# Optimization experiments

Measured on AMD Instinct MI355X. Metric: run time of the kernel, lower is better.

The kernel has to match this reference:

```python
import jax, jax.numpy as jnp
import numpy as np

L = 10      # LSTM layers
H = 128     # hidden size
ENC = 4096  # traffic_encoder_output_len
B = 8192    # batch
T = 12      # points_to_predict
NUM_MODES = 25


def setup_inputs() -> dict:
    key = jax.random.key(0)
    ks = jax.random.split(key, 10)
    s = 1.0 / np.sqrt(H)
    return {
        "backbone_encoded": jax.random.normal(ks[0], (B, ENC), jnp.float32),
        "fc_in_W": jax.random.normal(ks[1], (H, ENC), jnp.float32) / np.sqrt(ENC),
        "fc_in_b": jax.random.normal(ks[2], (H,), jnp.float32) * s,
        "Wih": jax.random.normal(ks[3], (L, 4 * H, H), jnp.float32) * s,
        "Whh": jax.random.normal(ks[4], (L, 4 * H, H), jnp.float32) * s,
        "bih": jax.random.normal(ks[5], (L, 4 * H), jnp.float32) * s,
        "bhh": jax.random.normal(ks[6], (L, 4 * H), jnp.float32) * s,
        "fc_out_W": jax.random.normal(ks[7], (3 * NUM_MODES, H), jnp.float32) * s,
        "fc_out_b": jax.random.normal(ks[8], (3 * NUM_MODES,), jnp.float32) * s,
        "points_to_predict": T,
    }


def _lstm_stack(x, Wih, Whh, bih, bhh):
    # x: [B, T, H]; PyTorch gate order: i, f, g, o
    def run_layer(x, l):
        def step(carry, xt):
            h, c = carry
            gates = xt @ Wih[l].T + h @ Whh[l].T + bih[l] + bhh[l]  # [B, 4H]
            i, f, g, o = jnp.split(gates, 4, axis=-1)
            c = jax.nn.sigmoid(f) * c + jax.nn.sigmoid(i) * jnp.tanh(g)
            h = jax.nn.sigmoid(o) * jnp.tanh(c)
            return (h, c), h
        b = x.shape[0]
        h0 = jnp.zeros((b, H), x.dtype)
        _, ys = jax.lax.scan(step, (h0, h0), jnp.swapaxes(x, 0, 1))  # [T, B, H]
        return jnp.swapaxes(ys, 0, 1)

    for l in range(L):
        x = run_layer(x, l)
    return x


def reference(backbone_encoded, fc_in_W, fc_in_b, Wih, Whh, bih, bhh,
              fc_out_W, fc_out_b, points_to_predict):
    enc = jax.nn.relu(backbone_encoded @ fc_in_W.T + fc_in_b)        # [B, H]
    x = jnp.repeat(enc[:, None, :], points_to_predict, axis=1)      # [B, T, H]
    y = _lstm_stack(x, Wih, Whh, bih, bhh)                           # [B, T, H]
    fc = y @ fc_out_W.T + fc_out_b                                   # [B, T, 75]
    b, t, _ = fc.shape
    # chunk(25, dim=channels) of consecutive pairs -> [B, 25, T, 2]
    predictions = fc[:, :, :50].reshape(b, t, NUM_MODES, 2).transpose(0, 2, 1, 3)
    probabilities = jax.nn.softmax(fc[:, -1, 50:], axis=-1)          # [B, 25]
    return predictions, probabilities
```

## Files before the change

### kernel.cpp

```cpp
#include <hip/hip_runtime.h>

typedef _Float16 h16;
typedef _Float16 h8 __attribute__((ext_vector_type(8)));
typedef float f4 __attribute__((ext_vector_type(4)));

#define NB 8192
#define NENC 4096
#define NH 128
#define NL 10
#define NT 12

#define OFF_FCIN 0
#define SZ_FCIN (128*4096)
#define OFF_W (OFF_FCIN + SZ_FCIN)
#define SZ_W (10*2*512*128)
#define OFF_FCOUT (OFF_W + SZ_W)
#define SZ_FCOUT (80*128)
#define OFF_ENC (OFF_FCOUT + SZ_FCOUT)
#define SZ_ENC (8192*128)
#define BYTE_BIAS ((OFF_ENC + SZ_ENC)*2)

__device__ __forceinline__ float sigf(float x) {
  float e = __builtin_amdgcn_exp2f(-1.4426950408889634f * x);
  return __builtin_amdgcn_rcpf(1.0f + e);
}
__device__ __forceinline__ float tanhf_(float x) {
  float e = __builtin_amdgcn_exp2f(-2.8853900817779268f * x);
  return 2.0f * __builtin_amdgcn_rcpf(1.0f + e) - 1.0f;
}
__device__ __forceinline__ f4 splat4(float v) { f4 r; r[0]=v; r[1]=v; r[2]=v; r[3]=v; return r; }
__device__ __forceinline__ h8 cvt8(float4 a, float4 b) {
  h8 r; r[0]=(h16)a.x; r[1]=(h16)a.y; r[2]=(h16)a.z; r[3]=(h16)a.w;
  r[4]=(h16)b.x; r[5]=(h16)b.y; r[6]=(h16)b.z; r[7]=(h16)b.w; return r;
}

__global__ __launch_bounds__(256) void prep(const float* __restrict__ fcinW,
                                            const float* __restrict__ Wih,
                                            const float* __restrict__ Whh,
                                            const float* __restrict__ bih,
                                            const float* __restrict__ bhh,
                                            const float* __restrict__ fcoutW,
                                            h16* __restrict__ wsh,
                                            float* __restrict__ wbias) {
  int idx = blockIdx.x * 256 + threadIdx.x;
  if (idx < 65536) {
    int r = idx >> 9, k8 = idx & 511;
    const float* src = fcinW + r * 4096 + k8 * 8;
    h8 v = cvt8(*(const float4*)src, *(const float4*)(src + 4));
    *(h8*)(wsh + OFF_FCIN + (((r >> 4) * 512 + k8) * 128 + (r & 15) * 8)) = v;
  } else if (idx < 229376) {
    int rel = idx - 65536;
    int l = rel >> 14, rr = rel & 16383;
    int ssel = rr >> 13, rk8 = rr & 8191;
    int r = rk8 >> 4, k8 = rk8 & 15;
    const float* src = (ssel ? Whh : Wih) + l * 65536 + r * 128 + k8 * 8;
    h8 v = cvt8(*(const float4*)src, *(const float4*)(src + 4));
    *(h8*)(wsh + OFF_W + (l * 2 + ssel) * 65536 +
           (((r >> 4) * 16 + k8) * 128 + (r & 15) * 8)) = v;
  } else if (idx < 230656) {
    int rel = idx - 229376;
    int r = rel >> 4, k8 = rel & 15;
    h8 v;
    if (r < 75) {
      const float* src = fcoutW + r * 128 + k8 * 8;
      v = cvt8(*(const float4*)src, *(const float4*)(src + 4));
    } else {
      for (int j = 0; j < 8; ++j) v[j] = (h16)0.f;
    }
    *(h8*)(wsh + OFF_FCOUT + (((r >> 4) * 16 + k8) * 128 + (r & 15) * 8)) = v;
  } else if (idx < 235776) {
    int rel = idx - 230656;
    wbias[rel] = bih[rel] + bhh[rel];
  }
}

__global__ __launch_bounds__(256) void kin(const float* __restrict__ A,
                                           const float* __restrict__ bvec,
                                           h16* __restrict__ wsh) {
  const h16* Wp = wsh + OFF_FCIN;
  h16* ench = wsh + OFF_ENC;
  int tid = threadIdx.x;
  int w = tid >> 6, lane = tid & 63, s = lane & 15, q = lane >> 4;
  int m0 = blockIdx.x * 16;
  int c0 = w * 32 + s, c1 = c0 + 16;
  f4 acc0 = splat4(bvec[c0]);
  f4 acc1 = splat4(bvec[c1]);
  const float* arow = A + (size_t)(m0 + s) * NENC;
  const h16* wp0 = Wp + (w * 2 + 0) * (512 * 128) + s * 8;
  const h16* wp1 = Wp + (w * 2 + 1) * (512 * 128) + s * 8;
#pragma unroll 4
  for (int kb = 0; kb < 128; ++kb) {
    int k0 = kb * 32 + q * 8;
    float4 x0 = *(const float4*)(arow + k0);
    float4 x1 = *(const float4*)(arow + k0 + 4);
    h8 af = cvt8(x0, x1);
    h8 b0 = *(const h8*)(wp0 + (kb * 4 + q) * 128);
    h8 b1 = *(const h8*)(wp1 + (kb * 4 + q) * 128);
    acc0 = __builtin_amdgcn_mfma_f32_16x16x32_f16(af, b0, acc0, 0, 0, 0);
    acc1 = __builtin_amdgcn_mfma_f32_16x16x32_f16(af, b1, acc1, 0, 0, 0);
  }
#pragma unroll
  for (int r = 0; r < 4; ++r) {
    int b = m0 + q * 4 + r;
    float v0 = acc0[r]; v0 = v0 > 0.f ? v0 : 0.f;
    float v1 = acc1[r]; v1 = v1 > 0.f ? v1 : 0.f;
    ench[(size_t)b * NH + c0] = (h16)v0;
    ench[(size_t)b * NH + c1] = (h16)v1;
  }
}

__global__ __launch_bounds__(512, 2) void lstm(h16* __restrict__ wsh,
                                               const float* __restrict__ wbias,
                                               const float* __restrict__ fcoutb,
                                               float* __restrict__ out) {
  __shared__ h16 xbuf[NT][32][136];
  __shared__ h16 hbuf[2][32][136];
  int tid = threadIdx.x;
  int w = tid >> 6, lane = tid & 63, s = lane & 15, q = lane >> 4;
  int brow = blockIdx.x * 32;
  const h16* ench = wsh + OFF_ENC;
  {
    int r = tid >> 4, cg = (tid & 15) * 8;
    h8 e = *(const h8*)(ench + (size_t)(brow + r) * NH + cg);
#pragma unroll
    for (int t = 0; t < NT; ++t) *(h8*)&xbuf[t][r][cg] = e;
  }
  h8 wx[4][4], wh[4][4];
  float bb[4];
  float c[2][4];
  for (int l = 0; l < NL; ++l) {
    const h16* wih = wsh + OFF_W + (l * 2 + 0) * 65536;
    const h16* whh = wsh + OFF_W + (l * 2 + 1) * 65536;
#pragma unroll
    for (int g = 0; g < 4; ++g) {
#pragma unroll
      for (int kt = 0; kt < 4; ++kt) {
        int off = (((g * 8 + w) * 16 + kt * 4 + q) * 128) + s * 8;
        wx[g][kt] = *(const h8*)(wih + off);
        wh[g][kt] = *(const h8*)(whh + off);
      }
      bb[g] = wbias[l * 512 + g * 128 + w * 16 + s];
    }
#pragma unroll
    for (int mt = 0; mt < 2; ++mt)
#pragma unroll
      for (int r = 0; r < 4; ++r) c[mt][r] = 0.f;
    for (int j = tid; j < 32 * 136 / 2; j += 512) ((unsigned int*)hbuf)[j] = 0u;
    __syncthreads();
    for (int t = 0; t < NT; ++t) {
      int cur = t & 1, nxt = cur ^ 1;
      f4 acc[4][2];
#pragma unroll
      for (int g = 0; g < 4; ++g)
#pragma unroll
        for (int mt = 0; mt < 2; ++mt) acc[g][mt] = splat4(bb[g]);
#pragma unroll
      for (int mt = 0; mt < 2; ++mt) {
        h8 ax[4], ah[4];
#pragma unroll
        for (int kt = 0; kt < 4; ++kt) {
          ax[kt] = *(const h8*)&xbuf[t][mt * 16 + s][kt * 32 + q * 8];
          ah[kt] = *(const h8*)&hbuf[cur][mt * 16 + s][kt * 32 + q * 8];
        }
#pragma unroll
        for (int g = 0; g < 4; ++g)
#pragma unroll
          for (int kt = 0; kt < 4; ++kt) {
            acc[g][mt] = __builtin_amdgcn_mfma_f32_16x16x32_f16(ax[kt], wx[g][kt], acc[g][mt], 0, 0, 0);
            acc[g][mt] = __builtin_amdgcn_mfma_f32_16x16x32_f16(ah[kt], wh[g][kt], acc[g][mt], 0, 0, 0);
          }
      }
      h16 hv[2][4];
#pragma unroll
      for (int mt = 0; mt < 2; ++mt)
#pragma unroll
        for (int r = 0; r < 4; ++r) {
          float iv = acc[0][mt][r], fv = acc[1][mt][r];
          float gv = acc[2][mt][r], ov = acc[3][mt][r];
          float cc = sigf(fv) * c[mt][r] + sigf(iv) * tanhf_(gv);
          c[mt][r] = cc;
          hv[mt][r] = (h16)(sigf(ov) * tanhf_(cc));
        }
      __syncthreads();
#pragma unroll
      for (int mt = 0; mt < 2; ++mt)
#pragma unroll
        for (int r = 0; r < 4; ++r) {
          int row = mt * 16 + q * 4 + r, col = w * 16 + s;
          xbuf[t][row][col] = hv[mt][r];
          hbuf[nxt][row][col] = hv[mt][r];
        }
      __syncthreads();
    }
  }
  h8 wo[5][4];
  float bo[5];
  const h16* fco = wsh + OFF_FCOUT;
#pragma unroll
  for (int nt = 0; nt < 5; ++nt) {
#pragma unroll
    for (int kt = 0; kt < 4; ++kt)
      wo[nt][kt] = *(const h8*)(fco + (nt * 16 + kt * 4 + q) * 128 + s * 8);
    int col = nt * 16 + s;
    bo[nt] = (col < 75) ? fcoutb[col] : 0.f;
  }
  float* probst = (float*)&hbuf[0][0][0];
  int tcount = (w < 4) ? 2 : 1;
  for (int ti = 0; ti < tcount; ++ti) {
    int t = w + ti * 8;
#pragma unroll
    for (int mt = 0; mt < 2; ++mt) {
      h8 ax[4];
#pragma unroll
      for (int kt = 0; kt < 4; ++kt)
        ax[kt] = *(const h8*)&xbuf[t][mt * 16 + s][kt * 32 + q * 8];
#pragma unroll
      for (int nt = 0; nt < 5; ++nt) {
        f4 a = splat4(bo[nt]);
#pragma unroll
        for (int kt = 0; kt < 4; ++kt)
          a = __builtin_amdgcn_mfma_f32_16x16x32_f16(ax[kt], wo[nt][kt], a, 0, 0, 0);
        int col = nt * 16 + s;
#pragma unroll
        for (int r = 0; r < 4; ++r) {
          int row = mt * 16 + q * 4 + r;
          int b = brow + row;
          float v = a[r];
          if (col < 50)
            out[(size_t)b * 600 + (col >> 1) * 24 + t * 2 + (col & 1)] = v;
          if (t == 11 && col >= 50 && col < 75)
            probst[row * 26 + (col - 50)] = v;
        }
      }
    }
  }
  __syncthreads();
  if (tid < 32) {
    float vals[25];
    float m = -1e30f;
#pragma unroll
    for (int j = 0; j < 25; ++j) { vals[j] = probst[tid * 26 + j]; m = vals[j] > m ? vals[j] : m; }
    float sum = 0.f;
#pragma unroll
    for (int j = 0; j < 25; ++j) {
      float e = __builtin_amdgcn_exp2f((vals[j] - m) * 1.4426950408889634f);
      vals[j] = e; sum += e;
    }
    float rs = 1.0f / sum;
    size_t pb = (size_t)4915200 + (size_t)(brow + tid) * 25;
#pragma unroll
    for (int j = 0; j < 25; ++j) out[pb + j] = vals[j] * rs;
  }
}

extern "C" void kernel_launch(void* const* d_in, const int* in_sizes, int n_in,
                              void* d_out, int out_size, void* d_ws, size_t ws_size,
                              hipStream_t stream) {
  const float* backbone = (const float*)d_in[0];
  const float* fcinW    = (const float*)d_in[1];
  const float* fcinb    = (const float*)d_in[2];
  const float* Wih      = (const float*)d_in[3];
  const float* Whh      = (const float*)d_in[4];
  const float* bih      = (const float*)d_in[5];
  const float* bhh      = (const float*)d_in[6];
  const float* fcoutW   = (const float*)d_in[7];
  const float* fcoutb   = (const float*)d_in[8];
  h16* wsh = (h16*)d_ws;
  float* wbias = (float*)((char*)d_ws + BYTE_BIAS);

  prep<<<922, 256, 0, stream>>>(fcinW, Wih, Whh, bih, bhh, fcoutW, wsh, wbias);
  kin<<<512, 256, 0, stream>>>(backbone, fcinb, wsh);
  lstm<<<256, 512, 0, stream>>>(wsh, wbias, fcoutb, (float*)d_out);
}
```

Before: 541.6 us.

## Precompute layer-0 input gates once and use a 13-slot LDS ring buffer

```diff
diff --git a/kernel.cpp b/kernel.cpp
--- a/kernel.cpp
+++ b/kernel.cpp
@@ -1,6 +1,7 @@
 #include <hip/hip_runtime.h>
 
 typedef _Float16 h16;
+typedef _Float16 h4 __attribute__((ext_vector_type(4)));
 typedef _Float16 h8 __attribute__((ext_vector_type(8)));
 typedef float f4 __attribute__((ext_vector_type(4)));
 
@@ -9,6 +10,7 @@
 #define NH 128
 #define NL 10
 #define NT 12
+#define PAD 136
 
 #define OFF_FCIN 0
 #define SZ_FCIN (128*4096)
@@ -18,7 +20,9 @@
 #define SZ_FCOUT (80*128)
 #define OFF_ENC (OFF_FCOUT + SZ_FCOUT)
 #define SZ_ENC (8192*128)
-#define BYTE_BIAS ((OFF_ENC + SZ_ENC)*2)
+#define OFF_GX0 (OFF_ENC + SZ_ENC)
+#define SZ_GX0 (8192*512)
+#define BYTE_BIAS ((OFF_GX0 + SZ_GX0)*2)
 
 __device__ __forceinline__ float sigf(float x) {
   float e = __builtin_amdgcn_exp2f(-1.4426950408889634f * x);
@@ -109,68 +113,91 @@
   }
 }
 
+__global__ __launch_bounds__(256) void kin2(h16* __restrict__ wsh,
+                                            const float* __restrict__ wbias) {
+  int tid = threadIdx.x;
+  int w2 = tid >> 6, lane = tid & 63, s = lane & 15, q = lane >> 4;
+  int bid = blockIdx.x;
+  int lb = bid >> 3, mt = (bid >> 2) & 1, cg = bid & 3;
+  const h16* ench = wsh + OFF_ENC;
+  const h16* wih0 = wsh + OFF_W;
+  h16* gx0 = wsh + OFF_GX0;
+  const h16* arow = ench + (size_t)(lb * 32 + mt * 16 + s) * NH;
+  h8 ax[4];
+#pragma unroll
+  for (int kt = 0; kt < 4; ++kt) ax[kt] = *(const h8*)(arow + kt * 32 + q * 8);
+#pragma unroll
+  for (int ti = 0; ti < 2; ++ti) {
+    int W = w2 * 2 + ti;
+    int rb = cg * 8 + W;
+    f4 acc = splat4(wbias[cg * 128 + W * 16 + s]);
+#pragma unroll
+    for (int kt = 0; kt < 4; ++kt) {
+      h8 b = *(const h8*)(wih0 + (rb * 16 + kt * 4 + q) * 128 + s * 8);
+      acc = __builtin_amdgcn_mfma_f32_16x16x32_f16(ax[kt], b, acc, 0, 0, 0);
+    }
+    h4 st; st[0] = (h16)acc[0]; st[1] = (h16)acc[1]; st[2] = (h16)acc[2]; st[3] = (h16)acc[3];
+    *(h4*)(gx0 + ((((size_t)lb * 8 + W) * 8 + cg * 2 + mt) * 64 + lane) * 4) = st;
+  }
+}
+
 __global__ __launch_bounds__(512, 2) void lstm(h16* __restrict__ wsh,
                                                const float* __restrict__ wbias,
                                                const float* __restrict__ fcoutb,
                                                float* __restrict__ out) {
-  __shared__ h16 xbuf[NT][32][136];
-  __shared__ h16 hbuf[2][32][136];
+  __shared__ h16 ring[13][32][PAD];
+  __shared__ float probst[32 * 26];
   int tid = threadIdx.x;
   int w = tid >> 6, lane = tid & 63, s = lane & 15, q = lane >> 4;
   int brow = blockIdx.x * 32;
-  const h16* ench = wsh + OFF_ENC;
-  {
-    int r = tid >> 4, cg = (tid & 15) * 8;
-    h8 e = *(const h8*)(ench + (size_t)(brow + r) * NH + cg);
-#pragma unroll
-    for (int t = 0; t < NT; ++t) *(h8*)&xbuf[t][r][cg] = e;
-  }
   h8 wx[4][4], wh[4][4];
   float bb[4];
   float c[2][4];
-  for (int l = 0; l < NL; ++l) {
-    const h16* wih = wsh + OFF_W + (l * 2 + 0) * 65536;
-    const h16* whh = wsh + OFF_W + (l * 2 + 1) * 65536;
-#pragma unroll
-    for (int g = 0; g < 4; ++g) {
-#pragma unroll
-      for (int kt = 0; kt < 4; ++kt) {
-        int off = (((g * 8 + w) * 16 + kt * 4 + q) * 128) + s * 8;
-        wx[g][kt] = *(const h8*)(wih + off);
-        wh[g][kt] = *(const h8*)(whh + off);
-      }
-      bb[g] = wbias[l * 512 + g * 128 + w * 16 + s];
-    }
+
+  {
+    const h16* whh = wsh + OFF_W + 65536;
+#pragma unroll
+    for (int g = 0; g < 4; ++g)
+#pragma unroll
+      for (int kt = 0; kt < 4; ++kt)
+        wh[g][kt] = *(const h8*)(whh + (((g * 8 + w) * 16 + kt * 4 + q) * 128) + s * 8);
+    f4 gx[4][2];
+    const h16* gxp = wsh + OFF_GX0 + ((size_t)blockIdx.x * 8 + w) * 8 * 256 + (size_t)lane * 4;
+#pragma unroll
+    for (int g = 0; g < 4; ++g)
+#pragma unroll
+      for (int mt = 0; mt < 2; ++mt) {
+        h4 v = *(const h4*)(gxp + (g * 2 + mt) * 256);
+        f4 a; a[0] = (float)v[0]; a[1] = (float)v[1]; a[2] = (float)v[2]; a[3] = (float)v[3];
+        gx[g][mt] = a;
+      }
 #pragma unroll
     for (int mt = 0; mt < 2; ++mt)
 #pragma unroll
       for (int r = 0; r < 4; ++r) c[mt][r] = 0.f;
-    for (int j = tid; j < 32 * 136 / 2; j += 512) ((unsigned int*)hbuf)[j] = 0u;
-    __syncthreads();
     for (int t = 0; t < NT; ++t) {
-      int cur = t & 1, nxt = cur ^ 1;
+      __syncthreads();
+      int rw = t + 11; if (rw >= 13) rw -= 13;
+      int rh = t + 10; if (rh >= 13) rh -= 13;
       f4 acc[4][2];
 #pragma unroll
       for (int g = 0; g < 4; ++g)
 #pragma unroll
-        for (int mt = 0; mt < 2; ++mt) acc[g][mt] = splat4(bb[g]);
-#pragma unroll
-      for (int mt = 0; mt < 2; ++mt) {
-        h8 ax[4], ah[4];
-#pragma unroll
-        for (int kt = 0; kt < 4; ++kt) {
-          ax[kt] = *(const h8*)&xbuf[t][mt * 16 + s][kt * 32 + q * 8];
-          ah[kt] = *(const h8*)&hbuf[cur][mt * 16 + s][kt * 32 + q * 8];
-        }
-#pragma unroll
-        for (int g = 0; g < 4; ++g)
-#pragma unroll
-          for (int kt = 0; kt < 4; ++kt) {
-            acc[g][mt] = __builtin_amdgcn_mfma_f32_16x16x32_f16(ax[kt], wx[g][kt], acc[g][mt], 0, 0, 0);
-            acc[g][mt] = __builtin_amdgcn_mfma_f32_16x16x32_f16(ah[kt], wh[g][kt], acc[g][mt], 0, 0, 0);
-          }
-      }
-      h16 hv[2][4];
+        for (int mt = 0; mt < 2; ++mt) acc[g][mt] = gx[g][mt];
+      if (t > 0) {
+#pragma unroll
+        for (int mt = 0; mt < 2; ++mt) {
+          h8 ah[4];
+#pragma unroll
+          for (int kt = 0; kt < 4; ++kt)
+            ah[kt] = *(const h8*)&ring[rh][mt * 16 + s][kt * 32 + q * 8];
+#pragma unroll
+          for (int g = 0; g < 4; ++g)
+#pragma unroll
+            for (int kt = 0; kt < 4; ++kt)
+              acc[g][mt] = __builtin_amdgcn_mfma_f32_16x16x32_f16(ah[kt], wh[g][kt], acc[g][mt], 0, 0, 0);
+        }
+      }
 #pragma unroll
       for (int mt = 0; mt < 2; ++mt)
 #pragma unroll
@@ -179,20 +206,77 @@
           float gv = acc[2][mt][r], ov = acc[3][mt][r];
           float cc = sigf(fv) * c[mt][r] + sigf(iv) * tanhf_(gv);
           c[mt][r] = cc;
-          hv[mt][r] = (h16)(sigf(ov) * tanhf_(cc));
-        }
+          ring[rw][mt * 16 + q * 4 + r][w * 16 + s] = (h16)(sigf(ov) * tanhf_(cc));
+        }
+    }
+  }
+  for (int l = 1; l < NL; ++l) {
+    const h16* wih = wsh + OFF_W + (size_t)(l * 2) * 65536;
+    const h16* whh = wih + 65536;
+#pragma unroll
+    for (int g = 0; g < 4; ++g) {
+#pragma unroll
+      for (int kt = 0; kt < 4; ++kt) {
+        int off = (((g * 8 + w) * 16 + kt * 4 + q) * 128) + s * 8;
+        wx[g][kt] = *(const h8*)(wih + off);
+        wh[g][kt] = *(const h8*)(whh + off);
+      }
+      bb[g] = wbias[l * 512 + g * 128 + w * 16 + s];
+    }
+#pragma unroll
+    for (int mt = 0; mt < 2; ++mt)
+#pragma unroll
+      for (int r = 0; r < 4; ++r) c[mt][r] = 0.f;
+    int base = 12 - l;
+    for (int t = 0; t < NT; ++t) {
       __syncthreads();
+      int rr = t + base; if (rr >= 13) rr -= 13;
+      int rw = rr - 1; if (rw < 0) rw += 13;
+      int rh = rw - 1; if (rh < 0) rh += 13;
+      f4 acc[4][2];
+#pragma unroll
+      for (int g = 0; g < 4; ++g)
+#pragma unroll
+        for (int mt = 0; mt < 2; ++mt) acc[g][mt] = splat4(bb[g]);
+#pragma unroll
+      for (int mt = 0; mt < 2; ++mt) {
+        h8 ax[4];
+#pragma unroll
+        for (int kt = 0; kt < 4; ++kt)
+          ax[kt] = *(const h8*)&ring[rr][mt * 16 + s][kt * 32 + q * 8];
+#pragma unroll
+        for (int g = 0; g < 4; ++g)
+#pragma unroll
+          for (int kt = 0; kt < 4; ++kt)
+            acc[g][mt] = __builtin_amdgcn_mfma_f32_16x16x32_f16(ax[kt], wx[g][kt], acc[g][mt], 0, 0, 0);
+      }
+      if (t > 0) {
+#pragma unroll
+        for (int mt = 0; mt < 2; ++mt) {
+          h8 ah[4];
+#pragma unroll
+          for (int kt = 0; kt < 4; ++kt)
+            ah[kt] = *(const h8*)&ring[rh][mt * 16 + s][kt * 32 + q * 8];
+#pragma unroll
+          for (int g = 0; g < 4; ++g)
+#pragma unroll
+            for (int kt = 0; kt < 4; ++kt)
+              acc[g][mt] = __builtin_amdgcn_mfma_f32_16x16x32_f16(ah[kt], wh[g][kt], acc[g][mt], 0, 0, 0);
+        }
+      }
 #pragma unroll
       for (int mt = 0; mt < 2; ++mt)
 #pragma unroll
         for (int r = 0; r < 4; ++r) {
-          int row = mt * 16 + q * 4 + r, col = w * 16 + s;
-          xbuf[t][row][col] = hv[mt][r];
-          hbuf[nxt][row][col] = hv[mt][r];
-        }
-      __syncthreads();
-    }
-  }
+          float iv = acc[0][mt][r], fv = acc[1][mt][r];
+          float gv = acc[2][mt][r], ov = acc[3][mt][r];
+          float cc = sigf(fv) * c[mt][r] + sigf(iv) * tanhf_(gv);
+          c[mt][r] = cc;
+          ring[rw][mt * 16 + q * 4 + r][w * 16 + s] = (h16)(sigf(ov) * tanhf_(cc));
+        }
+    }
+  }
+  __syncthreads();
   h8 wo[5][4];
   float bo[5];
   const h16* fco = wsh + OFF_FCOUT;
@@ -204,16 +288,16 @@
     int col = nt * 16 + s;
     bo[nt] = (col < 75) ? fcoutb[col] : 0.f;
   }
-  float* probst = (float*)&hbuf[0][0][0];
   int tcount = (w < 4) ? 2 : 1;
   for (int ti = 0; ti < tcount; ++ti) {
     int t = w + ti * 8;
+    int sl = t + 2; if (sl >= 13) sl -= 13;
 #pragma unroll
     for (int mt = 0; mt < 2; ++mt) {
       h8 ax[4];
 #pragma unroll
       for (int kt = 0; kt < 4; ++kt)
-        ax[kt] = *(const h8*)&xbuf[t][mt * 16 + s][kt * 32 + q * 8];
+        ax[kt] = *(const h8*)&ring[sl][mt * 16 + s][kt * 32 + q * 8];
 #pragma unroll
       for (int nt = 0; nt < 5; ++nt) {
         f4 a = splat4(bo[nt]);
@@ -270,5 +354,6 @@
 
   prep<<<922, 256, 0, stream>>>(fcinW, Wih, Whh, bih, bhh, fcoutW, wsh, wbias);
   kin<<<512, 256, 0, stream>>>(backbone, fcinb, wsh);
+  kin2<<<2048, 256, 0, stream>>>(wsh, wbias);
   lstm<<<256, 512, 0, stream>>>(wsh, wbias, fcoutb, (float*)d_out);
 }
```

Result: faster. 514.7 us (-5.0%).
